# Performance work log

Hardware: AMD Instinct MI355X
Metric: run time of the kernel (lower is better)

Reference implementation:

```python
import jax, jax.numpy as jnp
import numpy as np

C_SKIP = 64       # channels of a and of b (concat -> 128)
C_OUT = 64
N = 131072        # coarse nodes
E = 1048576       # directed edges (avg degree 8)
N_FINE = 4 * N    # fine mesh nodes after unpool
K = 3 * N_FINE    # unpool scatter assignments


def setup_inputs() -> dict:
    key = jax.random.key(0)
    ks = jax.random.split(key, 9)
    return {
        "a": jax.random.normal(ks[0], (C_SKIP, N), dtype=jnp.float32),
        "b": jax.random.normal(ks[1], (C_SKIP, N), dtype=jnp.float32),
        "W_self": jax.random.normal(ks[2], (C_OUT, 2 * C_SKIP), dtype=jnp.float32) * 0.05,
        "W_neigh": jax.random.normal(ks[3], (C_OUT, 2 * C_SKIP), dtype=jnp.float32) * 0.05,
        "bias": jax.random.normal(ks[4], (C_OUT,), dtype=jnp.float32) * 0.05,
        "gather_index": jax.random.randint(ks[5], (E,), 0, N),
        "reduce_index": jax.random.randint(ks[6], (E,), 0, N),
        "unpool_src": jax.random.randint(ks[7], (K,), 0, N),
        "unpool_dst": jax.random.randint(ks[8], (K,), 0, N_FINE),
    }


def reference(a, b, W_self, W_neigh, bias, gather_index, reduce_index, unpool_src, unpool_dst):
    # concat skip connection along channel dim (-2)
    x = jnp.concatenate((a, b), axis=-2)                  # [C_in, N]
    n = x.shape[-1]
    # GraphConv: gather source features along edges, segment-sum into targets
    msgs = x[:, gather_index]                              # [C_in, E]
    agg = jax.ops.segment_sum(msgs.T, reduce_index, num_segments=n).T  # [C_in, N]
    h = W_self @ x + W_neigh @ agg + bias[:, None]         # [C_out, N]
    h = jax.nn.relu(h)
    # GraphUnpool with reduce='amax': scatter-max coarse features to fine mesh
    out = jnp.zeros((h.shape[0], 4 * n), dtype=h.dtype)
    out = out.at[:, unpool_dst].max(h[:, unpool_src])      # [C_out, N_fine]
    return out
```

## Files before the change

### kernel.cpp

```cpp
#include <hip/hip_runtime.h>
#include <stdint.h>

constexpr int NN = 131072;
constexpr int EE = 1048576;
constexpr int NF = 4 * NN;
constexpr int KK = 3 * NF;

constexpr int NBLK = 64;
constexpr int TPS  = 1024;
constexpr int SH_E = 6;
constexpr int SH_K = 7;
constexpr int NB_E = NN >> SH_E;
constexpr int NB_K = NF >> SH_K;
constexpr int EPT_E = EE / NBLK / TPS;
constexpr int EPT_K = KK / NBLK / TPS;
constexpr int CAP_E = 2048;
constexpr int CAP_K = 1024;
constexpr int KOFF = NB_E * NBLK;
constexpr int NH   = NB_E * NBLK + NB_K * NBLK;
constexpr int NSCB = NH / 2048;
constexpr int NTRB = NN / 32 / 4;

typedef __attribute__((ext_vector_type(8))) short bf16x8;
typedef __attribute__((ext_vector_type(4))) float f32x4;

__device__ inline uint32_t bf16rn(float f) {
    uint32_t u = __float_as_uint(f);
    return (u + 0x7FFFu + ((u >> 16) & 1u)) >> 16;
}
__device__ inline uint32_t pack2(float lo, float hi) {
    return bf16rn(lo) | (bf16rn(hi) << 16);
}
__device__ inline float bf_lo(uint32_t v) { return __uint_as_float(v << 16); }
__device__ inline float bf_hi(uint32_t v) { return __uint_as_float(v & 0xFFFF0000u); }

template<int NB, int EPT>
__device__ void pass1_body(const int* __restrict__ idx, int shift,
                           int* __restrict__ histG, int blk, int* hist)
{
    for (int f = threadIdx.x; f < NB; f += TPS) hist[f] = 0;
    __syncthreads();
    int base = blk * (TPS * EPT);
#pragma unroll
    for (int u = 0; u < EPT; ++u) {
        int b = idx[base + u * TPS + threadIdx.x] >> shift;
        atomicAdd(&hist[b], 1);
    }
    __syncthreads();
    for (int f = threadIdx.x; f < NB; f += TPS)
        histG[f * NBLK + blk] = hist[f];
}

__global__ __launch_bounds__(1024) void k_fused1(
    const float* __restrict__ a, const float* __restrict__ b,
    uint32_t* __restrict__ xTb,
    const int* __restrict__ reduce_i, const int* __restrict__ up_dst,
    int* __restrict__ histG)
{
    __shared__ int smem[128 * 33];
    if (blockIdx.x < NTRB) {
        float (*tile)[33] = (float (*)[33])smem;
        for (int t = 0; t < 4; ++t) {
            int i0 = (blockIdx.x * 4 + t) * 32;
            for (int f = threadIdx.x; f < 128 * 32; f += TPS) {
                int c = f >> 5, j = f & 31;
                const float* src = (c < 64) ? a : b;
                tile[c][j] = src[(size_t)(c & 63) * NN + i0 + j];
            }
            __syncthreads();
            for (int f = threadIdx.x; f < 64 * 32; f += TPS) {
                int p = f & 63, j = f >> 6;
                xTb[(size_t)(i0 + j) * 64 + p] =
                    pack2(tile[2 * p][j], tile[2 * p + 1][j]);
            }
            __syncthreads();
        }
    } else if (blockIdx.x < NTRB + NBLK) {
        pass1_body<NB_E, EPT_E>(reduce_i, SH_E, histG, blockIdx.x - NTRB, smem);
    } else {
        pass1_body<NB_K, EPT_K>(up_dst, SH_K, histG + KOFF,
                                blockIdx.x - NTRB - NBLK, smem);
    }
}

__global__ __launch_bounds__(256) void k_bsum(
    const int* __restrict__ cnt, int* __restrict__ bsum)
{
    __shared__ int s[256];
    int base = blockIdx.x * 2048;
    int sum = 0;
    for (int j = threadIdx.x; j < 2048; j += 256) sum += cnt[base + j];
    s[threadIdx.x] = sum;
    __syncthreads();
    for (int o = 128; o > 0; o >>= 1) {
        if (threadIdx.x < o) s[threadIdx.x] += s[threadIdx.x + o];
        __syncthreads();
    }
    if (threadIdx.x == 0) bsum[blockIdx.x] = s[0];
}

__global__ __launch_bounds__(256) void k_final(
    int* __restrict__ offs, const int* __restrict__ bsum)
{
    __shared__ int ts[256];
    int partial = 0;
    for (int i = threadIdx.x; i < blockIdx.x; i += 256) partial += bsum[i];
    ts[threadIdx.x] = partial;
    __syncthreads();
    for (int o = 128; o > 0; o >>= 1) {
        if (threadIdx.x < o) ts[threadIdx.x] += ts[threadIdx.x + o];
        __syncthreads();
    }
    int bb = ts[0];
    __syncthreads();

    int base = blockIdx.x * 2048 + threadIdx.x * 8;
    int loc[8];
    int sum = 0;
#pragma unroll
    for (int u = 0; u < 8; ++u) {
        int v = offs[base + u];
        loc[u] = sum;
        sum += v;
    }
    ts[threadIdx.x] = sum;
    __syncthreads();
    for (int o = 1; o < 256; o <<= 1) {
        int v = (threadIdx.x >= o) ? ts[threadIdx.x - o] : 0;
        __syncthreads();
        ts[threadIdx.x] += v;
        __syncthreads();
    }
    int texc = (threadIdx.x == 0) ? 0 : ts[threadIdx.x - 1];
#pragma unroll
    for (int u = 0; u < 8; ++u) offs[base + u] = bb + texc + loc[u];
    if (blockIdx.x == gridDim.x - 1 && threadIdx.x == 255) offs[NH] = bb + ts[255];
}

template<int NB, int EPT>
__device__ void pass2_body(const int* __restrict__ idx,
                           const int* __restrict__ payload, int shift,
                           const int* __restrict__ offsG, int sub,
                           uint32_t* __restrict__ pairs, int blk, int* curs)
{
    for (int f = threadIdx.x; f < NB; f += TPS)
        curs[f] = offsG[f * NBLK + blk] - sub;
    __syncthreads();
    int lmask = (1 << shift) - 1;
    int base = blk * (TPS * EPT);
#pragma unroll
    for (int u = 0; u < EPT; ++u) {
        int e = base + u * TPS + threadIdx.x;
        int bk = idx[e];
        int pos = atomicAdd(&curs[bk >> shift], 1);
        pairs[pos] = (uint32_t)payload[e] | ((uint32_t)(bk & lmask) << 17);
    }
}

__global__ __launch_bounds__(1024) void k_pass2(
    const int* __restrict__ reduce_i, const int* __restrict__ gather_i,
    const int* __restrict__ up_dst, const int* __restrict__ up_src,
    const int* __restrict__ offs,
    uint32_t* __restrict__ pairsE, uint32_t* __restrict__ pairsK)
{
    __shared__ int curs[NB_K];
    if (blockIdx.x < NBLK)
        pass2_body<NB_E, EPT_E>(reduce_i, gather_i, SH_E, offs, 0,
                                pairsE, blockIdx.x, curs);
    else
        pass2_body<NB_K, EPT_K>(up_dst, up_src, SH_K, offs + KOFF, EE,
                                pairsK, blockIdx.x - NBLK, curs);
}

__global__ __launch_bounds__(256) void k_aggcsr(
    const uint32_t* __restrict__ xTb, const int* __restrict__ offsE,
    const uint32_t* __restrict__ pairsE, uint32_t* __restrict__ aggB)
{
    __shared__ uint32_t list[CAP_E];
    __shared__ int offs[65];
    __shared__ int curs[64];
    __shared__ int cnt_s;
    int bin = blockIdx.x;
    if (threadIdx.x == 0) {
        int beg = offsE[bin * NBLK];
        cnt_s = min(offsE[(bin + 1) * NBLK] - beg, CAP_E);
    }
    if (threadIdx.x < 64) curs[threadIdx.x] = 0;
    __syncthreads();
    int beg = offsE[bin * NBLK];
    int cnt = cnt_s;
    for (int i = threadIdx.x; i < cnt; i += 256)
        atomicAdd(&curs[(pairsE[beg + i] >> 17) & 63], 1);
    __syncthreads();
    if (threadIdx.x == 0) {
        int run = 0;
        for (int j = 0; j < 64; ++j) {
            offs[j] = run;
            run += curs[j];
            curs[j] = offs[j];
        }
        offs[64] = run;
    }
    __syncthreads();
    for (int i = threadIdx.x; i < cnt; i += 256) {
        uint32_t u = pairsE[beg + i];
        int p = atomicAdd(&curs[(u >> 17) & 63], 1);
        list[p] = u;
    }
    __syncthreads();

    int w = threadIdx.x >> 6, lane = threadIdx.x & 63;
    int n0 = w * 16, n1 = n0 + 16;
    int e0 = offs[n0], e1 = offs[n1];
    size_t rowbase = (size_t)(bin * 64) * 64 + lane;
    float sx = 0.f, sy = 0.f;
    int cur = n0;
    for (int e = e0; e < e1; e += 16) {
        int nb = e1 - e;
        uint32_t pr[16], v[16];
#pragma unroll
        for (int j = 0; j < 16; ++j)
            pr[j] = list[e + ((j < nb) ? j : (nb - 1))];
#pragma unroll
        for (int j = 0; j < 16; ++j)
            v[j] = xTb[(size_t)(pr[j] & 0x1FFFF) * 64 + lane];
#pragma unroll
        for (int j = 0; j < 16; ++j) {
            if (j < nb) {
                int d = (pr[j] >> 17) & 63;
                if (d != cur) {
                    aggB[rowbase + (size_t)cur * 64] = pack2(sx, sy);
                    for (int z = cur + 1; z < d; ++z)
                        aggB[rowbase + (size_t)z * 64] = 0u;
                    cur = d;
                    sx = 0.f; sy = 0.f;
                }
                sx += bf_lo(v[j]);
                sy += bf_hi(v[j]);
            }
        }
    }
    aggB[rowbase + (size_t)cur * 64] = pack2(sx, sy);
    for (int z = cur + 1; z < n1; ++z)
        aggB[rowbase + (size_t)z * 64] = 0u;
}

__global__ __launch_bounds__(256) void k_gemm(
    const uint32_t* __restrict__ xTb, const uint32_t* __restrict__ aggB,
    const float* __restrict__ Wself, const float* __restrict__ Wneigh,
    const float* __restrict__ bias, uint32_t* __restrict__ hT)
{
    int lane = threadIdx.x & 63;
    int wid = blockIdx.x * 4 + (threadIdx.x >> 6);
    int lr = lane & 15, lq = lane >> 4;

    bf16x8 wf[4][8];
#pragma unroll
    for (int mt = 0; mt < 4; ++mt) {
#pragma unroll
        for (int kt = 0; kt < 8; ++kt) {
            const float* W = (kt < 4) ? Wself : Wneigh;
            const float* p = W + (size_t)(mt * 16 + lr) * 128 + (kt & 3) * 32 + lq * 8;
            bf16x8 v;
#pragma unroll
            for (int j = 0; j < 8; ++j) v[j] = (short)bf16rn(p[j]);
            wf[mt][kt] = v;
        }
    }
    float bv[4][4];
#pragma unroll
    for (int mt = 0; mt < 4; ++mt)
#pragma unroll
        for (int r = 0; r < 4; ++r)
            bv[mt][r] = bias[mt * 16 + lq * 4 + r];

    const int NG = NN / 16;
    int stride = gridDim.x * 4;
    for (int g = wid; g < NG; g += stride) {
        int n = g * 16 + lr;
        const uint32_t* xr = xTb + (size_t)n * 64 + lq * 4;
        const uint32_t* ar = aggB + (size_t)n * 64 + lq * 4;
        bf16x8 bq[8];
#pragma unroll
        for (int kt = 0; kt < 4; ++kt)
            bq[kt] = *reinterpret_cast<const bf16x8*>(xr + kt * 16);
#pragma unroll
        for (int kt = 0; kt < 4; ++kt)
            bq[4 + kt] = *reinterpret_cast<const bf16x8*>(ar + kt * 16);
#pragma unroll
        for (int mt = 0; mt < 4; ++mt) {
            f32x4 acc = {0.f, 0.f, 0.f, 0.f};
#pragma unroll
            for (int kt = 0; kt < 8; ++kt)
                acc = __builtin_amdgcn_mfma_f32_16x16x32_bf16(wf[mt][kt], bq[kt], acc, 0, 0, 0);
            uint32_t u0 = pack2(fmaxf(acc[0] + bv[mt][0], 0.f), fmaxf(acc[1] + bv[mt][1], 0.f));
            uint32_t u1 = pack2(fmaxf(acc[2] + bv[mt][2], 0.f), fmaxf(acc[3] + bv[mt][3], 0.f));
            *reinterpret_cast<uint2*>(hT + (size_t)n * 32 + mt * 8 + lq * 2) = make_uint2(u0, u1);
        }
    }
}

__global__ __launch_bounds__(256) void k_unpoolcsr(
    const uint16_t* __restrict__ hT16, const int* __restrict__ offsK,
    const uint32_t* __restrict__ pairsK, float* __restrict__ out)
{
    __shared__ uint32_t list[CAP_K];
    __shared__ int offs[129];
    __shared__ int curs[128];
    __shared__ uint16_t buf[128][65];
    __shared__ int cnt_s;
    int bin = blockIdx.x;
    if (threadIdx.x == 0) {
        int beg = offsK[bin * NBLK] - EE;
        cnt_s = min(offsK[(bin + 1) * NBLK] - EE - beg, CAP_K);
    }
    if (threadIdx.x < 128) curs[threadIdx.x] = 0;
    for (int f = threadIdx.x; f < 128 * 65; f += 256) ((uint16_t*)buf)[f] = 0;
    __syncthreads();
    int beg = offsK[bin * NBLK] - EE;
    int cnt = cnt_s;
    for (int i = threadIdx.x; i < cnt; i += 256)
        atomicAdd(&curs[(pairsK[beg + i] >> 17) & 127], 1);
    __syncthreads();
    if (threadIdx.x == 0) {
        int run = 0;
        for (int j = 0; j < 128; ++j) {
            offs[j] = run;
            run += curs[j];
            curs[j] = offs[j];
        }
        offs[128] = run;
    }
    __syncthreads();
    for (int i = threadIdx.x; i < cnt; i += 256) {
        uint32_t u = pairsK[beg + i];
        int p = atomicAdd(&curs[(u >> 17) & 127], 1);
        list[p] = u;
    }
    __syncthreads();

    int w = threadIdx.x >> 6, lane = threadIdx.x & 63;
    int n0 = w * 32, n1 = n0 + 32;
    int e0 = offs[n0], e1 = offs[n1];
    uint32_t m = 0;
    int cur = n0;
    for (int e = e0; e < e1; e += 16) {
        int nb = e1 - e;
        uint32_t pr[16], v[16];
#pragma unroll
        for (int j = 0; j < 16; ++j)
            pr[j] = list[e + ((j < nb) ? j : (nb - 1))];
#pragma unroll
        for (int j = 0; j < 16; ++j)
            v[j] = hT16[(size_t)(pr[j] & 0x1FFFF) * 64 + lane];
#pragma unroll
        for (int j = 0; j < 16; ++j) {
            if (j < nb) {
                int d = (pr[j] >> 17) & 127;
                if (d != cur) {
                    buf[cur][lane] = (uint16_t)m;
                    cur = d;
                    m = 0;
                }
                m = max(m, v[j]);
            }
        }
    }
    buf[cur][lane] = (uint16_t)m;
    __syncthreads();
    int j0 = bin << 7;
    for (int f = threadIdx.x; f < 64 * 128; f += 256) {
        int c = f >> 7, j = f & 127;
        out[(size_t)c * NF + j0 + j] = __uint_as_float(((uint32_t)buf[j][c]) << 16);
    }
}

extern "C" void kernel_launch(void* const* d_in, const int* in_sizes, int n_in,
                              void* d_out, int out_size, void* d_ws, size_t ws_size,
                              hipStream_t stream)
{
    const float* a      = (const float*)d_in[0];
    const float* b      = (const float*)d_in[1];
    const float* Wself  = (const float*)d_in[2];
    const float* Wneigh = (const float*)d_in[3];
    const float* bias   = (const float*)d_in[4];
    const int* gather_i = (const int*)d_in[5];
    const int* reduce_i = (const int*)d_in[6];
    const int* up_src   = (const int*)d_in[7];
    const int* up_dst   = (const int*)d_in[8];
    float* out = (float*)d_out;

    uint32_t* xTb   = (uint32_t*)d_ws;
    uint32_t* aggB  = xTb + (size_t)NN * 64;
    uint32_t* hT    = aggB + (size_t)NN * 64;
    uint32_t* pairsK= hT + (size_t)NN * 32;
    int* offs       = (int*)(pairsK + KK);
    int* bsum       = offs + (size_t)NH + 1;
    uint32_t* pairsE= hT;

    size_t need = ((size_t)NN * 160 + KK + (size_t)NH + 1 + NSCB) * 4;
    if (ws_size < need) return;

    k_fused1<<<NTRB + 2 * NBLK, TPS, 0, stream>>>(a, b, xTb, reduce_i, up_dst, offs);

    k_bsum<<<NSCB, 256, 0, stream>>>(offs, bsum);
    k_final<<<NSCB, 256, 0, stream>>>(offs, bsum);

    k_pass2<<<2 * NBLK, TPS, 0, stream>>>(reduce_i, gather_i, up_dst, up_src,
                                          offs, pairsE, pairsK);

    k_aggcsr<<<NB_E, 256, 0, stream>>>(xTb, offs, pairsE, aggB);

    k_gemm<<<512, 256, 0, stream>>>(xTb, aggB, Wself, Wneigh, bias, hT);

    k_unpoolcsr<<<NB_K, 256, 0, stream>>>((const uint16_t*)hT, offs + KOFF,
                                          pairsK, out);
}
```

Baseline: 272.2 us.

## Coarsen radix binning and filter sub-bins in consumer kernels via ballot compaction

The counting-sort passes now bin by coarser keys (512 nodes for edges, 1024 fine nodes for unpool), and the pass1/pass2 kernels run 256 blocks instead of 64 per index stream. This cuts the number of histogram entries per block and makes each pass2 block handle fewer elements. The aggregation and unpool kernels now launch 8 blocks per coarse bin. Each block scans the whole coarse bin, keeps only its sub-bin's entries using wave ballot compaction into shared memory, and then does the same local sort as before. The trade-off is that every consumer block rereads its coarse bin 8 times, and shared memory capacity drops, which raises the risk of truncating dense bins.

```diff
diff --git a/kernel.cpp b/kernel.cpp
--- a/kernel.cpp
+++ b/kernel.cpp
@@ -6,20 +6,21 @@
 constexpr int NF = 4 * NN;
 constexpr int KK = 3 * NF;
 
-constexpr int NBLK = 64;
+constexpr int NSB  = 256;
 constexpr int TPS  = 1024;
-constexpr int SH_E = 6;
-constexpr int SH_K = 7;
-constexpr int NB_E = NN >> SH_E;
-constexpr int NB_K = NF >> SH_K;
-constexpr int EPT_E = EE / NBLK / TPS;
-constexpr int EPT_K = KK / NBLK / TPS;
-constexpr int CAP_E = 2048;
-constexpr int CAP_K = 1024;
-constexpr int KOFF = NB_E * NBLK;
-constexpr int NH   = NB_E * NBLK + NB_K * NBLK;
-constexpr int NSCB = NH / 2048;
-constexpr int NTRB = NN / 32 / 4;
+constexpr int SHC_E = 9;
+constexpr int SHC_K = 10;
+constexpr int NBC_E = NN >> SHC_E;
+constexpr int NBC_K = NF >> SHC_K;
+constexpr int EPT_E = EE / NSB / TPS;
+constexpr int EPT_K = KK / NSB / TPS;
+constexpr int KOFF2 = NBC_E * NSB;
+constexpr int NH2   = KOFF2 + NBC_K * NSB;
+constexpr int NSCB  = NH2 / 2048;
+constexpr int NTRB  = NN / 32 / 4;
+
+constexpr int CAP_AG = 1024;
+constexpr int CAP_UP = 896;
 
 typedef __attribute__((ext_vector_type(8))) short bf16x8;
 typedef __attribute__((ext_vector_type(4))) float f32x4;
@@ -48,7 +49,7 @@
     }
     __syncthreads();
     for (int f = threadIdx.x; f < NB; f += TPS)
-        histG[f * NBLK + blk] = hist[f];
+        histG[f * NSB + blk] = hist[f];
 }
 
 __global__ __launch_bounds__(1024) void k_fused1(
@@ -75,11 +76,11 @@
             }
             __syncthreads();
         }
-    } else if (blockIdx.x < NTRB + NBLK) {
-        pass1_body<NB_E, EPT_E>(reduce_i, SH_E, histG, blockIdx.x - NTRB, smem);
+    } else if (blockIdx.x < NTRB + NSB) {
+        pass1_body<NBC_E, EPT_E>(reduce_i, SHC_E, histG, blockIdx.x - NTRB, smem);
     } else {
-        pass1_body<NB_K, EPT_K>(up_dst, SH_K, histG + KOFF,
-                                blockIdx.x - NTRB - NBLK, smem);
+        pass1_body<NBC_K, EPT_K>(up_dst, SHC_K, histG + KOFF2,
+                                 blockIdx.x - NTRB - NSB, smem);
     }
 }
 
@@ -134,7 +135,7 @@
     int texc = (threadIdx.x == 0) ? 0 : ts[threadIdx.x - 1];
 #pragma unroll
     for (int u = 0; u < 8; ++u) offs[base + u] = bb + texc + loc[u];
-    if (blockIdx.x == gridDim.x - 1 && threadIdx.x == 255) offs[NH] = bb + ts[255];
+    if (blockIdx.x == gridDim.x - 1 && threadIdx.x == 255) offs[NH2] = bb + ts[255];
 }
 
 template<int NB, int EPT>
@@ -143,10 +144,10 @@
                            const int* __restrict__ offsG, int sub,
                            uint32_t* __restrict__ pairs, int blk, int* curs)
 {
+    int lmask = (1 << shift) - 1;
     for (int f = threadIdx.x; f < NB; f += TPS)
-        curs[f] = offsG[f * NBLK + blk] - sub;
-    __syncthreads();
-    int lmask = (1 << shift) - 1;
+        curs[f] = offsG[f * NSB + blk] - sub;
+    __syncthreads();
     int base = blk * (TPS * EPT);
 #pragma unroll
     for (int u = 0; u < EPT; ++u) {
@@ -163,56 +164,78 @@
     const int* __restrict__ offs,
     uint32_t* __restrict__ pairsE, uint32_t* __restrict__ pairsK)
 {
-    __shared__ int curs[NB_K];
-    if (blockIdx.x < NBLK)
-        pass2_body<NB_E, EPT_E>(reduce_i, gather_i, SH_E, offs, 0,
-                                pairsE, blockIdx.x, curs);
+    __shared__ int curs[NBC_K];
+    if (blockIdx.x < NSB)
+        pass2_body<NBC_E, EPT_E>(reduce_i, gather_i, SHC_E, offs, 0,
+                                 pairsE, blockIdx.x, curs);
     else
-        pass2_body<NB_K, EPT_K>(up_dst, up_src, SH_K, offs + KOFF, EE,
-                                pairsK, blockIdx.x - NBLK, curs);
+        pass2_body<NBC_K, EPT_K>(up_dst, up_src, SHC_K, offs + KOFF2, EE,
+                                 pairsK, blockIdx.x - NSB, curs);
 }
 
 __global__ __launch_bounds__(256) void k_aggcsr(
-    const uint32_t* __restrict__ xTb, const int* __restrict__ offsE,
+    const uint32_t* __restrict__ xTb, const int* __restrict__ offs,
     const uint32_t* __restrict__ pairsE, uint32_t* __restrict__ aggB)
 {
-    __shared__ uint32_t list[CAP_E];
-    __shared__ int offs[65];
+    __shared__ uint32_t stage[CAP_AG];
+    __shared__ uint32_t list[CAP_AG];
+    __shared__ int loffs[65];
     __shared__ int curs[64];
-    __shared__ int cnt_s;
-    int bin = blockIdx.x;
-    if (threadIdx.x == 0) {
-        int beg = offsE[bin * NBLK];
-        cnt_s = min(offsE[(bin + 1) * NBLK] - beg, CAP_E);
-    }
+    __shared__ int nstage;
+    int binc = blockIdx.x >> 3, sub = blockIdx.x & 7;
+    int beg = offs[binc * NSB], end = offs[(binc + 1) * NSB];
+    if (threadIdx.x == 0) nstage = 0;
     if (threadIdx.x < 64) curs[threadIdx.x] = 0;
     __syncthreads();
-    int beg = offsE[bin * NBLK];
-    int cnt = cnt_s;
+    int lane = threadIdx.x & 63;
+
+    for (int i0 = beg; i0 < end; i0 += 256) {
+        int i = i0 + threadIdx.x;
+        bool mine = false;
+        uint32_t ent = 0;
+        if (i < end) {
+            uint32_t u = pairsE[i];
+            int loc = u >> 17;
+            mine = (loc >> 6) == sub;
+            ent = (u & 0x1FFFFu) | ((uint32_t)(loc & 63) << 17);
+        }
+        unsigned long long mask = __ballot(mine);
+        if (mask) {
+            int leader = __ffsll(mask) - 1;
+            int rank = __popcll(mask & ((1ull << lane) - 1ull));
+            int wb = 0;
+            if (lane == leader) wb = atomicAdd(&nstage, (int)__popcll(mask));
+            wb = __shfl(wb, leader);
+            int p = wb + rank;
+            if (mine && p < CAP_AG) stage[p] = ent;
+        }
+    }
+    __syncthreads();
+    int cnt = min(nstage, CAP_AG);
     for (int i = threadIdx.x; i < cnt; i += 256)
-        atomicAdd(&curs[(pairsE[beg + i] >> 17) & 63], 1);
+        atomicAdd(&curs[stage[i] >> 17], 1);
     __syncthreads();
     if (threadIdx.x == 0) {
         int run = 0;
         for (int j = 0; j < 64; ++j) {
-            offs[j] = run;
+            loffs[j] = run;
             run += curs[j];
-            curs[j] = offs[j];
-        }
-        offs[64] = run;
+            curs[j] = loffs[j];
+        }
+        loffs[64] = run;
     }
     __syncthreads();
     for (int i = threadIdx.x; i < cnt; i += 256) {
-        uint32_t u = pairsE[beg + i];
-        int p = atomicAdd(&curs[(u >> 17) & 63], 1);
+        uint32_t u = stage[i];
+        int p = atomicAdd(&curs[u >> 17], 1);
         list[p] = u;
     }
     __syncthreads();
 
-    int w = threadIdx.x >> 6, lane = threadIdx.x & 63;
+    int w = threadIdx.x >> 6;
     int n0 = w * 16, n1 = n0 + 16;
-    int e0 = offs[n0], e1 = offs[n1];
-    size_t rowbase = (size_t)(bin * 64) * 64 + lane;
+    int e0 = loffs[n0], e1 = loffs[n1];
+    size_t rowbase = (size_t)(binc * 512 + sub * 64) * 64 + lane;
     float sx = 0.f, sy = 0.f;
     int cur = n0;
     for (int e = e0; e < e1; e += 16) {
@@ -227,7 +250,7 @@
 #pragma unroll
         for (int j = 0; j < 16; ++j) {
             if (j < nb) {
-                int d = (pr[j] >> 17) & 63;
+                int d = pr[j] >> 17;
                 if (d != cur) {
                     aggB[rowbase + (size_t)cur * 64] = pack2(sx, sy);
                     for (int z = cur + 1; z < d; ++z)
@@ -304,44 +327,66 @@
     const uint16_t* __restrict__ hT16, const int* __restrict__ offsK,
     const uint32_t* __restrict__ pairsK, float* __restrict__ out)
 {
-    __shared__ uint32_t list[CAP_K];
-    __shared__ int offs[129];
+    __shared__ uint32_t stage[CAP_UP];
+    __shared__ uint32_t list[CAP_UP];
+    __shared__ int loffs[129];
     __shared__ int curs[128];
     __shared__ uint16_t buf[128][65];
-    __shared__ int cnt_s;
-    int bin = blockIdx.x;
-    if (threadIdx.x == 0) {
-        int beg = offsK[bin * NBLK] - EE;
-        cnt_s = min(offsK[(bin + 1) * NBLK] - EE - beg, CAP_K);
-    }
+    __shared__ int nstage;
+    int binc = blockIdx.x >> 3, sub = blockIdx.x & 7;
+    int beg = offsK[binc * NSB] - EE, end = offsK[(binc + 1) * NSB] - EE;
+    if (threadIdx.x == 0) nstage = 0;
     if (threadIdx.x < 128) curs[threadIdx.x] = 0;
     for (int f = threadIdx.x; f < 128 * 65; f += 256) ((uint16_t*)buf)[f] = 0;
     __syncthreads();
-    int beg = offsK[bin * NBLK] - EE;
-    int cnt = cnt_s;
+    int lane = threadIdx.x & 63;
+
+    for (int i0 = beg; i0 < end; i0 += 256) {
+        int i = i0 + threadIdx.x;
+        bool mine = false;
+        uint32_t ent = 0;
+        if (i < end) {
+            uint32_t u = pairsK[i];
+            int loc = u >> 17;
+            mine = (loc >> 7) == sub;
+            ent = (u & 0x1FFFFu) | ((uint32_t)(loc & 127) << 17);
+        }
+        unsigned long long mask = __ballot(mine);
+        if (mask) {
+            int leader = __ffsll(mask) - 1;
+            int rank = __popcll(mask & ((1ull << lane) - 1ull));
+            int wb = 0;
+            if (lane == leader) wb = atomicAdd(&nstage, (int)__popcll(mask));
+            wb = __shfl(wb, leader);
+            int p = wb + rank;
+            if (mine && p < CAP_UP) stage[p] = ent;
+        }
+    }
+    __syncthreads();
+    int cnt = min(nstage, CAP_UP);
     for (int i = threadIdx.x; i < cnt; i += 256)
-        atomicAdd(&curs[(pairsK[beg + i] >> 17) & 127], 1);
+        atomicAdd(&curs[stage[i] >> 17], 1);
     __syncthreads();
     if (threadIdx.x == 0) {
         int run = 0;
         for (int j = 0; j < 128; ++j) {
-            offs[j] = run;
+            loffs[j] = run;
             run += curs[j];
-            curs[j] = offs[j];
-        }
-        offs[128] = run;
+            curs[j] = loffs[j];
+        }
+        loffs[128] = run;
     }
     __syncthreads();
     for (int i = threadIdx.x; i < cnt; i += 256) {
-        uint32_t u = pairsK[beg + i];
-        int p = atomicAdd(&curs[(u >> 17) & 127], 1);
+        uint32_t u = stage[i];
+        int p = atomicAdd(&curs[u >> 17], 1);
         list[p] = u;
     }
     __syncthreads();
 
-    int w = threadIdx.x >> 6, lane = threadIdx.x & 63;
+    int w = threadIdx.x >> 6;
     int n0 = w * 32, n1 = n0 + 32;
-    int e0 = offs[n0], e1 = offs[n1];
+    int e0 = loffs[n0], e1 = loffs[n1];
     uint32_t m = 0;
     int cur = n0;
     for (int e = e0; e < e1; e += 16) {
@@ -356,7 +401,7 @@
 #pragma unroll
         for (int j = 0; j < 16; ++j) {
             if (j < nb) {
-                int d = (pr[j] >> 17) & 127;
+                int d = pr[j] >> 17;
                 if (d != cur) {
                     buf[cur][lane] = (uint16_t)m;
                     cur = d;
@@ -368,7 +413,7 @@
     }
     buf[cur][lane] = (uint16_t)m;
     __syncthreads();
-    int j0 = bin << 7;
+    int j0 = binc * 1024 + sub * 128;
     for (int f = threadIdx.x; f < 64 * 128; f += 256) {
         int c = f >> 7, j = f & 127;
         out[(size_t)c * NF + j0 + j] = __uint_as_float(((uint32_t)buf[j][c]) << 16);
@@ -395,24 +440,24 @@
     uint32_t* hT    = aggB + (size_t)NN * 64;
     uint32_t* pairsK= hT + (size_t)NN * 32;
     int* offs       = (int*)(pairsK + KK);
-    int* bsum       = offs + (size_t)NH + 1;
+    int* bsum       = offs + (size_t)NH2 + 1;
     uint32_t* pairsE= hT;
 
-    size_t need = ((size_t)NN * 160 + KK + (size_t)NH + 1 + NSCB) * 4;
+    size_t need = ((size_t)NN * 160 + KK + (size_t)NH2 + 1 + NSCB) * 4;
     if (ws_size < need) return;
 
-    k_fused1<<<NTRB + 2 * NBLK, TPS, 0, stream>>>(a, b, xTb, reduce_i, up_dst, offs);
+    k_fused1<<<NTRB + 2 * NSB, TPS, 0, stream>>>(a, b, xTb, reduce_i, up_dst, offs);
 
     k_bsum<<<NSCB, 256, 0, stream>>>(offs, bsum);
     k_final<<<NSCB, 256, 0, stream>>>(offs, bsum);
 
-    k_pass2<<<2 * NBLK, TPS, 0, stream>>>(reduce_i, gather_i, up_dst, up_src,
-                                          offs, pairsE, pairsK);
-
-    k_aggcsr<<<NB_E, 256, 0, stream>>>(xTb, offs, pairsE, aggB);
+    k_pass2<<<2 * NSB, TPS, 0, stream>>>(reduce_i, gather_i, up_dst, up_src,
+                                         offs, pairsE, pairsK);
+
+    k_aggcsr<<<8 * NBC_E, 256, 0, stream>>>(xTb, offs, pairsE, aggB);
 
     k_gemm<<<512, 256, 0, stream>>>(xTb, aggB, Wself, Wneigh, bias, hT);
 
-    k_unpoolcsr<<<NB_K, 256, 0, stream>>>((const uint16_t*)hT, offs + KOFF,
-                                          pairsK, out);
-}
+    k_unpoolcsr<<<8 * NBC_K, 256, 0, stream>>>((const uint16_t*)hT, offs + KOFF2,
+                                               pairsK, out);
+}
```

Result: faster. 243.3 us, median of 2 (-10.6%).
